# Kernel tuning notes

Measured on AMD Instinct MI355X. Metric: run time of the kernel, lower is better.

The kernel has to match this reference:

```python
import jax, jax.numpy as jnp
import numpy as np


def setup_inputs() -> dict:
    key = jax.random.key(0)
    kx, = jax.random.split(key, 1)
    B, H, W = 4, 256, 256
    x = jax.random.normal(kx, (B, H, W), dtype=jnp.float32)
    # learned scalar params per build(): b init zero, w1 init one, w2 init zero
    # use small random-ish nonzero values so w2 path is exercised
    b = jnp.array([0.1], dtype=jnp.float32)
    w1 = jnp.array([1.0], dtype=jnp.float32)
    w2 = jnp.array([0.5], dtype=jnp.float32)
    return {"x": x, "b": b, "w1": w1, "w2": w2}


def reference(x, b, w1, w2):
    # Original: for i in range(W): t_i = concat(x[:,:,:i], x[:,:,:W-i])
    # i.e. t_i[..., j] = x[..., j] if j < i else x[..., j - i]  (Toeplitz-like shift)
    # out[:, i] = x * w1 + (b - t_i) * w2 ; out shape (B, W, H, W)
    W = x.shape[2]
    jj = jnp.arange(W)[None, :]          # (1, W) column index j
    ii = jnp.arange(W)[:, None]          # (W, 1) shift index i
    idx = jnp.where(jj < ii, jj, jj - ii)  # (W, W) gather indices
    t = x[:, :, idx]                     # (B, H, W_i, W_j)
    t = jnp.transpose(t, (0, 2, 1, 3))   # (B, W_i, H, W_j)
    return x[:, None, :, :] * w1[0] + (b[0] - t) * w2[0]
```

## Files before the change

kernel.cpp:

```cpp
#include <hip/hip_runtime.h>


__global__ __launch_bounds__(256) void overlap_kernel(
    const float* __restrict__ x,
    const float* __restrict__ bp,
    const float* __restrict__ w1p,
    const float* __restrict__ w2p,
    float* __restrict__ out) {
  const float bb = bp[0];
  const float w1 = w1p[0];
  const float w2 = w2p[0];

  int tid  = blockIdx.x * 256 + threadIdx.x;
  int lane = threadIdx.x & 63;
  int j0   = lane << 2;
  int h    = (tid >> 6) & 255;
  int i0   = (tid >> 14) & 31;

  #pragma unroll
  for (int nn = 0; nn < 4; ++nn) {
    const float* __restrict__ xrow = x + (((nn << 8) + h) << 8);
    float4 a = *reinterpret_cast<const float4*>(xrow + j0);

    #pragma unroll
    for (int ii = 0; ii < 8; ++ii) {
      int i = i0 + (ii << 5);
      int q = i >> 2;
      int r = i & 3;
      int srcA = lane - q;
      int srcB = srcA - 1;

      float Ax = __shfl(a.x, srcA, 64);
      float Ay = __shfl(a.y, srcA, 64);
      float Az = __shfl(a.z, srcA, 64);
      float Aw = __shfl(a.w, srcA, 64);
      float Bx = __shfl(a.x, srcB, 64);
      float By = __shfl(a.y, srcB, 64);
      float Bz = __shfl(a.z, srcB, 64);
      float Bw = __shfl(a.w, srcB, 64);
      (void)Bx;

      float s0, s1, s2, s3;
      if (r == 0)      { s0 = Ax; s1 = Ay; s2 = Az; s3 = Aw; }
      else if (r == 1) { s0 = Bw; s1 = Ax; s2 = Ay; s3 = Az; }
      else if (r == 2) { s0 = Bz; s1 = Bw; s2 = Ax; s3 = Ay; }
      else             { s0 = By; s1 = Bz; s2 = Bw; s3 = Ax; }

      float t0 = (j0 + 0 < i) ? a.x : s0;
      float t1 = (j0 + 1 < i) ? a.y : s1;
      float t2 = (j0 + 2 < i) ? a.z : s2;
      float t3 = (j0 + 3 < i) ? a.w : s3;

      float4 o;
      o.x = a.x * w1 + (bb - t0) * w2;
      o.y = a.y * w1 + (bb - t1) * w2;
      o.z = a.z * w1 + (bb - t2) * w2;
      o.w = a.w * w1 + (bb - t3) * w2;

      size_t f4 = (((size_t)(((nn << 8) + i) << 8) + h) << 6) + lane;
      reinterpret_cast<float4*>(out)[f4] = o;
    }
  }
}

extern "C" void kernel_launch(void* const* d_in, const int* in_sizes, int n_in,
                              void* d_out, int out_size, void* d_ws, size_t ws_size,
                              hipStream_t stream) {
  const float* x  = (const float*)d_in[0];
  const float* b  = (const float*)d_in[1];
  const float* w1 = (const float*)d_in[2];
  const float* w2 = (const float*)d_in[3];
  float* out = (float*)d_out;

  int blocks = out_size / (256 * 128);
  overlap_kernel<<<blocks, 256, 0, stream>>>(x, b, w1, w2, out);
}
```

Baseline: 47.31 us.

## Make shift index block-uniform and specialize shuffle pattern per remainder

Reassigns work so each block handles a single shift index i, a single batch element and 32 rows of H, making q, r and the j<i masks uniform per block. A template over r = i&3 selects at compile time which four shuffles are needed, replacing eight shuffles plus a runtime select chain. Each thread now reloads x rows (eight loads for eight stores) instead of reusing one loaded row for eight shifts, which raises input read traffic that should mostly hit cache. The grid is fixed at 8192 blocks.

Measured after the change: 46.50 us, median of 2. Within noise of the previous version (-1.7%).

```diff
diff --git a/kernel.cpp b/kernel.cpp
--- a/kernel.cpp
+++ b/kernel.cpp
@@ -1,5 +1,46 @@
 #include <hip/hip_runtime.h>
 
+
+template <int R>
+__device__ __forceinline__ void run_rows(
+    const float4* __restrict__ xin,
+    float4* __restrict__ oout,
+    int srcA, int srcB,
+    bool c0, bool c1, bool c2, bool c3,
+    float w1, float w2, float bb) {
+  #pragma unroll
+  for (int it = 0; it < 8; ++it) {
+    float4 a = xin[it * 64];
+
+    float s0, s1, s2, s3;
+    if constexpr (R == 0) {
+      s0 = __shfl(a.x, srcA, 64); s1 = __shfl(a.y, srcA, 64);
+      s2 = __shfl(a.z, srcA, 64); s3 = __shfl(a.w, srcA, 64);
+    } else if constexpr (R == 1) {
+      s0 = __shfl(a.w, srcB, 64); s1 = __shfl(a.x, srcA, 64);
+      s2 = __shfl(a.y, srcA, 64); s3 = __shfl(a.z, srcA, 64);
+    } else if constexpr (R == 2) {
+      s0 = __shfl(a.z, srcB, 64); s1 = __shfl(a.w, srcB, 64);
+      s2 = __shfl(a.x, srcA, 64); s3 = __shfl(a.y, srcA, 64);
+    } else {
+      s0 = __shfl(a.y, srcB, 64); s1 = __shfl(a.z, srcB, 64);
+      s2 = __shfl(a.w, srcB, 64); s3 = __shfl(a.x, srcA, 64);
+    }
+
+    float t0 = c0 ? a.x : s0;
+    float t1 = c1 ? a.y : s1;
+    float t2 = c2 ? a.z : s2;
+    float t3 = c3 ? a.w : s3;
+
+    float4 o;
+    o.x = a.x * w1 + (bb - t0) * w2;
+    o.y = a.y * w1 + (bb - t1) * w2;
+    o.z = a.z * w1 + (bb - t2) * w2;
+    o.w = a.w * w1 + (bb - t3) * w2;
+
+    oout[it * 64] = o;
+  }
+}
 
 __global__ __launch_bounds__(256) void overlap_kernel(
     const float* __restrict__ x,
@@ -11,55 +52,35 @@
   const float w1 = w1p[0];
   const float w2 = w2p[0];
 
-  int tid  = blockIdx.x * 256 + threadIdx.x;
-  int lane = threadIdx.x & 63;
-  int j0   = lane << 2;
-  int h    = (tid >> 6) & 255;
-  int i0   = (tid >> 14) & 31;
+  int bl = blockIdx.x;
+  int hc = bl & 7;
+  int i  = (bl >> 3) & 255;
+  int n  = bl >> 11;
 
-  #pragma unroll
-  for (int nn = 0; nn < 4; ++nn) {
-    const float* __restrict__ xrow = x + (((nn << 8) + h) << 8);
-    float4 a = *reinterpret_cast<const float4*>(xrow + j0);
+  int lane  = threadIdx.x & 63;
+  int w     = threadIdx.x >> 6;
+  int hbase = (hc << 5) + (w << 3);
+  int j0    = lane << 2;
 
-    #pragma unroll
-    for (int ii = 0; ii < 8; ++ii) {
-      int i = i0 + (ii << 5);
-      int q = i >> 2;
-      int r = i & 3;
-      int srcA = lane - q;
-      int srcB = srcA - 1;
+  int q = i >> 2;
+  int r = i & 3;
+  int srcA = lane - q;
+  int srcB = srcA - 1;
 
-      float Ax = __shfl(a.x, srcA, 64);
-      float Ay = __shfl(a.y, srcA, 64);
-      float Az = __shfl(a.z, srcA, 64);
-      float Aw = __shfl(a.w, srcA, 64);
-      float Bx = __shfl(a.x, srcB, 64);
-      float By = __shfl(a.y, srcB, 64);
-      float Bz = __shfl(a.z, srcB, 64);
-      float Bw = __shfl(a.w, srcB, 64);
-      (void)Bx;
+  bool c0 = (j0 + 0) < i;
+  bool c1 = (j0 + 1) < i;
+  bool c2 = (j0 + 2) < i;
+  bool c3 = (j0 + 3) < i;
 
-      float s0, s1, s2, s3;
-      if (r == 0)      { s0 = Ax; s1 = Ay; s2 = Az; s3 = Aw; }
-      else if (r == 1) { s0 = Bw; s1 = Ax; s2 = Ay; s3 = Az; }
-      else if (r == 2) { s0 = Bz; s1 = Bw; s2 = Ax; s3 = Ay; }
-      else             { s0 = By; s1 = Bz; s2 = Bw; s3 = Ax; }
+  const float4* xin = reinterpret_cast<const float4*>(x + (n << 16) + (hbase << 8)) + lane;
+  float4* oout = reinterpret_cast<float4*>(out) +
+                 (((n << 8) + i) << 14) + (hbase << 6) + lane;
 
-      float t0 = (j0 + 0 < i) ? a.x : s0;
-      float t1 = (j0 + 1 < i) ? a.y : s1;
-      float t2 = (j0 + 2 < i) ? a.z : s2;
-      float t3 = (j0 + 3 < i) ? a.w : s3;
-
-      float4 o;
-      o.x = a.x * w1 + (bb - t0) * w2;
-      o.y = a.y * w1 + (bb - t1) * w2;
-      o.z = a.z * w1 + (bb - t2) * w2;
-      o.w = a.w * w1 + (bb - t3) * w2;
-
-      size_t f4 = (((size_t)(((nn << 8) + i) << 8) + h) << 6) + lane;
-      reinterpret_cast<float4*>(out)[f4] = o;
-    }
+  switch (r) {
+    case 0: run_rows<0>(xin, oout, srcA, srcB, c0, c1, c2, c3, w1, w2, bb); break;
+    case 1: run_rows<1>(xin, oout, srcA, srcB, c0, c1, c2, c3, w1, w2, bb); break;
+    case 2: run_rows<2>(xin, oout, srcA, srcB, c0, c1, c2, c3, w1, w2, bb); break;
+    default: run_rows<3>(xin, oout, srcA, srcB, c0, c1, c2, c3, w1, w2, bb); break;
   }
 }
 
@@ -72,6 +93,5 @@
   const float* w2 = (const float*)d_in[3];
   float* out = (float*)d_out;
 
-  int blocks = out_size / (256 * 128);
-  overlap_kernel<<<blocks, 256, 0, stream>>>(x, b, w1, w2, out);
+  overlap_kernel<<<8192, 256, 0, stream>>>(x, b, w1, w2, out);
 }
```
